# Performance work log

Hardware: AMD Instinct MI355X
Metric: run time of the kernel (lower is better)

The kernel has to match this reference:

```python
import jax, jax.numpy as jnp
import numpy as np

# ---- constants matching the torch module / entmax normmax_bisect defaults ----
ALPHA = 5.0                 # normmax alpha (entmax normmax_bisect default)
N_BISECT = 50               # bisection iterations
K_EXP = 1.0 / (ALPHA - 1.0)        # p_i propto (z_i - tau)_+^{1/(alpha-1)}
AK_EXP = ALPHA / (ALPHA - 1.0)     # norm condition: sum (z-tau)_+^{alpha/(alpha-1)} = 1
EPS = 1e-8                  # module epsilon
LN_EPS = 1e-5               # torch LayerNorm default eps

B, N, C, D = 32, 1024, 64, 768


def _bisect_tau(z):
    # z: [..., S]; find tau with f(tau) = sum_i relu(z_i - tau)^AK_EXP - 1 = 0 (f decreasing)
    max_val = jnp.max(z, axis=-1, keepdims=True)
    lo, hi = max_val - 1.0, max_val  # f(lo) >= 0, f(hi) = -1 < 0

    def body(_, carry):
        lo, hi = carry
        tau = 0.5 * (lo + hi)
        f = jnp.sum(jnp.maximum(z - tau, 0.0) ** AK_EXP, axis=-1, keepdims=True) - 1.0
        lo = jnp.where(f >= 0, tau, lo)
        hi = jnp.where(f >= 0, hi, tau)
        return (lo, hi)

    lo, hi = jax.lax.fori_loop(0, N_BISECT, body, (lo, hi))
    return 0.5 * (lo + hi)


def normmax_last(z):
    # normmax over last axis: p = s / sum(s), s = relu(z - tau)^{1/(alpha-1)}, ||s||_alpha = 1
    tau = _bisect_tau(z)
    u = jnp.maximum(z - tau, 0.0)
    u_safe = jnp.where(u > 0, u, 1.0)
    s = jnp.where(u > 0, u_safe ** K_EXP, 0.0)
    return s / jnp.sum(s, axis=-1, keepdims=True)


def layernorm(x, scale, bias):
    mu = jnp.mean(x, axis=-1, keepdims=True)
    var = jnp.mean((x - mu) ** 2, axis=-1, keepdims=True)
    return (x - mu) * jax.lax.rsqrt(var + LN_EPS) * scale + bias


def setup_inputs() -> dict:
    key = jax.random.key(0)
    ks = jax.random.split(key, 10)
    w = lambda k, shp: (jax.random.normal(k, shp, dtype=jnp.float32) * 0.02)
    return {
        "features": jax.random.normal(ks[0], (B, N, D), dtype=jnp.float32),
        "slots_init": jax.random.normal(ks[1], (B, C, D), dtype=jnp.float32),
        "mask": jax.random.randint(ks[2], (B, N), 0, 2, dtype=jnp.int32),
        "ln_f_scale": jnp.ones((D,), jnp.float32),
        "ln_f_bias": jnp.zeros((D,), jnp.float32),
        "ln_s_scale": jnp.ones((D,), jnp.float32),
        "ln_s_bias": jnp.zeros((D,), jnp.float32),
        "Wk": w(ks[3], (D, D)),
        "Wv": w(ks[4], (D, D)),
        "Wq": w(ks[5], (D, D)),
        "W_ih": w(ks[6], (3 * D, D)),
        "W_hh": w(ks[7], (3 * D, D)),
        "b_ih": jnp.zeros((3 * D,), jnp.float32),
        "b_hh": jnp.zeros((3 * D,), jnp.float32),
    }


def reference(features, slots_init, mask, ln_f_scale, ln_f_bias, ln_s_scale, ln_s_bias,
              Wk, Wv, Wq, W_ih, W_hh, b_ih, b_hh):
    f = layernorm(features, ln_f_scale, ln_f_bias)        # [B,N,D]
    k = f @ Wk.T
    v = f @ Wv.T
    b, n, d = v.shape
    c = slots_init.shape[1]
    m = mask[:, None, :] != 0                             # [B,1,N], broadcasts over C

    # num_iterations = 1; straight-through (detach trick) is the identity here.
    slots_prev = slots_init
    s = layernorm(slots_init, ln_s_scale, ln_s_bias)
    q = s @ Wq.T                                          # [B,C,D]
    logits = jnp.einsum('bcd,bnd->bcn', q, k) * (1.0 / np.sqrt(d))
    logits = jnp.where(m, logits, 0.0)                    # masked_fill(mask==0, 0)
    # normmax over the slot axis (dim=1)
    attn = jnp.moveaxis(normmax_last(jnp.moveaxis(logits, 1, -1)), -1, 1)  # [B,C,N]
    attn = jnp.where(m, attn, 0.0)
    attn_wm = attn / (jnp.sum(attn, axis=-1, keepdims=True) + EPS)
    updates = jnp.einsum('bcn,bnd->bcd', attn_wm, v)      # [B,C,D]

    # torch GRUCell: r,z,n gate order
    x = updates.reshape(-1, d)
    h = slots_prev.reshape(-1, d)
    gi = x @ W_ih.T + b_ih
    gh = h @ W_hh.T + b_hh
    ir, iz, in_ = jnp.split(gi, 3, axis=-1)
    hr, hz, hn = jnp.split(gh, 3, axis=-1)
    r = jax.nn.sigmoid(ir + hr)
    zg = jax.nn.sigmoid(iz + hz)
    ng = jnp.tanh(in_ + r * hn)
    h_new = (1.0 - zg) * ng + zg * h
    slots = h_new.reshape(b, c, d)
    return slots, attn
```

## Files before the change

kernel.cpp:

```cpp
#include <hip/hip_runtime.h>
#include <cstdint>
#include <cmath>

#define DEVINL __device__ __forceinline__

using f32x4  = __attribute__((ext_vector_type(4))) float;
using bf16x8 = __attribute__((ext_vector_type(8))) __bf16;
using u16x8  = __attribute__((ext_vector_type(8))) unsigned short;
using u16x4  = __attribute__((ext_vector_type(4))) unsigned short;
using fl4    = __attribute__((ext_vector_type(4))) float;

DEVINL float bf2f(unsigned short h) {
    unsigned int u = ((unsigned int)h) << 16;
    float f; __builtin_memcpy(&f, &u, 4); return f;
}
DEVINL unsigned short f2bf(float f) {
    unsigned int u; __builtin_memcpy(&u, &f, 4);
    u += 0x7FFFu + ((u >> 16) & 1u);
    return (unsigned short)(u >> 16);
}
DEVINL float sqrt_raw(float x) {
    float r; asm("v_sqrt_f32 %0, %1" : "=v"(r) : "v"(x)); return r;
}

DEVINL void gload_lds16(const unsigned short* g, unsigned short* l) {
    __builtin_amdgcn_global_load_lds(
        (__attribute__((address_space(1))) void*)g,
        (__attribute__((address_space(3))) void*)l,
        16, 0, 0);
}

__global__ __launch_bounds__(256)
void tr2_f2b_split(const float* __restrict__ Wq, const float* __restrict__ Wk,
                   unsigned short* __restrict__ WqT_hi, unsigned short* __restrict__ WqT_lo,
                   unsigned short* __restrict__ WkT_hi, unsigned short* __restrict__ WkT_lo)
{
    constexpr int S = 768 * 768;
    const int o = blockIdx.x * 256 + threadIdx.x;
    if (o >= 2 * S) return;
    const float* x; unsigned short *yh, *yl; int i;
    if (o < S) { x = Wq; yh = WqT_hi; yl = WqT_lo; i = o; }
    else       { x = Wk; yh = WkT_hi; yl = WkT_lo; i = o - S; }
    const int e = i / 768, d = i - e * 768;
    const float v = x[d * 768 + e];
    const unsigned short h = f2bf(v);
    yh[i] = h;
    yl[i] = f2bf(v - bf2f(h));
}

__global__ __launch_bounds__(256)
void conv2_fused(const float* __restrict__ Wih, const float* __restrict__ Whh,
                 const float* __restrict__ sl,  const float* __restrict__ Wv,
                 unsigned short* __restrict__ Wihb, unsigned short* __restrict__ Whhb,
                 unsigned short* __restrict__ slb,  unsigned short* __restrict__ Wvb)
{
    constexpr int S1 = 3 * 768 * 768;
    constexpr int S2 = S1 + 3 * 768 * 768;
    constexpr int S3 = S2 + 32 * 64 * 768;
    constexpr int S4 = S3 + 768 * 768;
    const int i = (blockIdx.x * 256 + threadIdx.x) * 4;
    if (i >= S4) return;
    const float* src; unsigned short* dst; int off;
    if (i < S1)      { src = Wih; dst = Wihb; off = i; }
    else if (i < S2) { src = Whh; dst = Whhb; off = i - S1; }
    else if (i < S3) { src = sl;  dst = slb;  off = i - S2; }
    else             { src = Wv;  dst = Wvb;  off = i - S3; }
    fl4 v = *(const fl4*)(src + off);
    u16x4 o;
#pragma unroll
    for (int j = 0; j < 4; ++j) o[j] = f2bf(v[j]);
    *(u16x4*)(dst + off) = o;
}

template<int BM, int BN, int WAVES_M, int WAVES_N, int OUTMODE>
__global__ __launch_bounds__(256)
void gemm_bt3(const unsigned short* __restrict__ Ah, const unsigned short* __restrict__ Al,
              const unsigned short* __restrict__ Bh, const unsigned short* __restrict__ Bl,
              void* __restrict__ out1, unsigned short* __restrict__ out2,
              int N, int K, long sA, long sB, long sC, float alpha)
{
    constexpr int BK = 32;
    constexpr int WM = BM / WAVES_M, WN = BN / WAVES_N;
    constexpr int MT = WM / 16, NT = WN / 16;
    __shared__ alignas(16) unsigned short Ash[BM * BK], Asl[BM * BK];
    __shared__ alignas(16) unsigned short Bsh[BN * BK], Bsl[BN * BK];

    const int bz = blockIdx.z;
    Ah += (long)bz * sA; Al += (long)bz * sA;
    Bh += (long)bz * sB; Bl += (long)bz * sB;
    const int row0 = blockIdx.y * BM, col0 = blockIdx.x * BN;
    const int tid = threadIdx.x, l = tid & 63, w = tid >> 6;
    const int wm = w / WAVES_N, wn = w % WAVES_N;
    const int fr = l & 15, fq = l >> 4;

    f32x4 acc[MT][NT] = {};
    constexpr int ACALLS = (BM * BK) / (256 * 8);
    constexpr int BCALLS = (BN * BK) / (256 * 8);

    for (int kt = 0; kt < K; kt += BK) {
#pragma unroll
        for (int c = 0; c < ACALLS; ++c) {
            const int e = (c * 256 + tid) * 8;
            const long g = (long)(row0 + (e >> 5)) * K + kt + (e & 31);
            gload_lds16(Ah + g, &Ash[e]);
            gload_lds16(Al + g, &Asl[e]);
        }
#pragma unroll
        for (int c = 0; c < BCALLS; ++c) {
            const int e = (c * 256 + tid) * 8;
            const long g = (long)(col0 + (e >> 5)) * K + kt + (e & 31);
            gload_lds16(Bh + g, &Bsh[e]);
            gload_lds16(Bl + g, &Bsl[e]);
        }
        __syncthreads();

        bf16x8 afh[MT], afl[MT], bfh[NT], bfl[NT];
#pragma unroll
        for (int m = 0; m < MT; ++m) {
            const int o = (wm * WM + m * 16 + fr) * BK + fq * 8;
            afh[m] = __builtin_bit_cast(bf16x8, *(const u16x8*)&Ash[o]);
            afl[m] = __builtin_bit_cast(bf16x8, *(const u16x8*)&Asl[o]);
        }
#pragma unroll
        for (int n = 0; n < NT; ++n) {
            const int o = (wn * WN + n * 16 + fr) * BK + fq * 8;
            bfh[n] = __builtin_bit_cast(bf16x8, *(const u16x8*)&Bsh[o]);
            bfl[n] = __builtin_bit_cast(bf16x8, *(const u16x8*)&Bsl[o]);
        }
#pragma unroll
        for (int m = 0; m < MT; ++m)
#pragma unroll
            for (int n = 0; n < NT; ++n) {
                acc[m][n] = __builtin_amdgcn_mfma_f32_16x16x32_bf16(afh[m], bfh[n], acc[m][n], 0, 0, 0);
                acc[m][n] = __builtin_amdgcn_mfma_f32_16x16x32_bf16(afh[m], bfl[n], acc[m][n], 0, 0, 0);
                acc[m][n] = __builtin_amdgcn_mfma_f32_16x16x32_bf16(afl[m], bfh[n], acc[m][n], 0, 0, 0);
            }
        __syncthreads();
    }

#pragma unroll
    for (int m = 0; m < MT; ++m) {
        const int gr = row0 + wm * WM + m * 16 + fq * 4;
#pragma unroll
        for (int n = 0; n < NT; ++n) {
            const int gc = col0 + wn * WN + n * 16 + fr;
#pragma unroll
            for (int j = 0; j < 4; ++j) {
                const float v = acc[m][n][j] * alpha;
                const long idx = (long)bz * sC + (long)(gr + j) * N + gc;
                if (OUTMODE == 0) {
                    ((float*)out1)[idx] = v;
                } else {
                    const unsigned short h = f2bf(v);
                    ((unsigned short*)out1)[idx] = h;
                    out2[idx] = f2bf(v - bf2f(h));
                }
            }
        }
    }
}

template<int BM, int BN, int WAVES_M, int WAVES_N, bool OUT_F32>
__global__ __launch_bounds__(256)
void gemm_bt(const unsigned short* __restrict__ A,
             const unsigned short* __restrict__ B,
             void* __restrict__ Cv,
             int N, int K, long sA, long sB, long sC, float alpha)
{
    constexpr int BK = 32;
    constexpr int WM = BM / WAVES_M, WN = BN / WAVES_N;
    constexpr int MT = WM / 16, NT = WN / 16;
    __shared__ alignas(16) unsigned short As[BM * BK];
    __shared__ alignas(16) unsigned short Bs[BN * BK];

    const int bz = blockIdx.z;
    A += (long)bz * sA;
    B += (long)bz * sB;
    const int row0 = blockIdx.y * BM, col0 = blockIdx.x * BN;
    const int tid = threadIdx.x, l = tid & 63, w = tid >> 6;
    const int wm = w / WAVES_N, wn = w % WAVES_N;
    const int fr = l & 15, fq = l >> 4;

    f32x4 acc[MT][NT] = {};
    constexpr int ACALLS = (BM * BK) / (256 * 8);
    constexpr int BCALLS = (BN * BK) / (256 * 8);

    for (int kt = 0; kt < K; kt += BK) {
#pragma unroll
        for (int c = 0; c < ACALLS; ++c) {
            const int e = (c * 256 + tid) * 8;
            gload_lds16(A + (long)(row0 + (e >> 5)) * K + kt + (e & 31), &As[e]);
        }
#pragma unroll
        for (int c = 0; c < BCALLS; ++c) {
            const int e = (c * 256 + tid) * 8;
            gload_lds16(B + (long)(col0 + (e >> 5)) * K + kt + (e & 31), &Bs[e]);
        }
        __syncthreads();

        bf16x8 af[MT], bfr[NT];
#pragma unroll
        for (int m = 0; m < MT; ++m)
            af[m] = __builtin_bit_cast(bf16x8, *(const u16x8*)&As[(wm * WM + m * 16 + fr) * BK + fq * 8]);
#pragma unroll
        for (int n = 0; n < NT; ++n)
            bfr[n] = __builtin_bit_cast(bf16x8, *(const u16x8*)&Bs[(wn * WN + n * 16 + fr) * BK + fq * 8]);
#pragma unroll
        for (int m = 0; m < MT; ++m)
#pragma unroll
            for (int n = 0; n < NT; ++n)
                acc[m][n] = __builtin_amdgcn_mfma_f32_16x16x32_bf16(af[m], bfr[n], acc[m][n], 0, 0, 0);
        __syncthreads();
    }

#pragma unroll
    for (int m = 0; m < MT; ++m) {
        const int gr = row0 + wm * WM + m * 16 + fq * 4;
#pragma unroll
        for (int n = 0; n < NT; ++n) {
            const int gc = col0 + wn * WN + n * 16 + fr;
#pragma unroll
            for (int j = 0; j < 4; ++j) {
                const float v = acc[m][n][j] * alpha;
                if (OUT_F32) ((float*)Cv)[(long)bz * sC + (long)(gr + j) * N + gc] = v;
                else ((unsigned short*)Cv)[(long)bz * sC + (long)(gr + j) * N + gc] = f2bf(v);
            }
        }
    }
}

template<int BM, int BN, int WAVES_M, int WAVES_N>
__global__ __launch_bounds__(256)
void gemm_nt_rs(const unsigned short* __restrict__ A,
                const unsigned short* __restrict__ Bm,
                unsigned short* __restrict__ C,
                int N, int K, long sA, long sB, long sC)
{
    constexpr int BK = 32;
    constexpr int WM = BM / WAVES_M, WN = BN / WAVES_N;
    constexpr int MT = WM / 16, NT = WN / 16;
    __shared__ alignas(16) unsigned short As[BM * BK];
    __shared__ alignas(16) unsigned short Bs[BN * BK];
    __shared__ float rsums[BM];

    const int bz = blockIdx.z;
    A += (long)bz * sA;
    Bm += (long)bz * sB;
    const int row0 = blockIdx.y * BM, col0 = blockIdx.x * BN;
    const int tid = threadIdx.x, l = tid & 63, w = tid >> 6;
    const int wm = w / WAVES_N, wn = w % WAVES_N;
    const int fr = l & 15, fq = l >> 4;

    f32x4 acc[MT][NT] = {};
    float rsum = 0.f;
    constexpr int ACALLS = (BM * BK) / (256 * 8);
    constexpr int TPR = BN / 8;
    constexpr int RPP = 256 / TPR;
    const int br = tid / TPR, bc8 = (tid % TPR) * 8;

    for (int kt = 0; kt < K; kt += BK) {
#pragma unroll
        for (int c = 0; c < ACALLS; ++c) {
            const int e = (c * 256 + tid) * 8;
            gload_lds16(A + (long)(row0 + (e >> 5)) * K + kt + (e & 31), &As[e]);
        }
#pragma unroll
        for (int p = 0; p < BK / RPP; ++p) {
            const int r = p * RPP + br;
            u16x8 vv = *(const u16x8*)(Bm + (long)(kt + r) * N + col0 + bc8);
#pragma unroll
            for (int j = 0; j < 8; ++j) Bs[(bc8 + j) * BK + r] = vv[j];
        }
        __syncthreads();

        if (tid < BM) {
#pragma unroll
            for (int kk = 0; kk < BK / 8; ++kk) {
                u16x8 vv = *(const u16x8*)&As[tid * BK + kk * 8];
#pragma unroll
                for (int j = 0; j < 8; ++j) rsum += bf2f(vv[j]);
            }
        }

        bf16x8 af[MT], bfr[NT];
#pragma unroll
        for (int m = 0; m < MT; ++m)
            af[m] = __builtin_bit_cast(bf16x8, *(const u16x8*)&As[(wm * WM + m * 16 + fr) * BK + fq * 8]);
#pragma unroll
        for (int n = 0; n < NT; ++n)
            bfr[n] = __builtin_bit_cast(bf16x8, *(const u16x8*)&Bs[(wn * WN + n * 16 + fr) * BK + fq * 8]);
#pragma unroll
        for (int m = 0; m < MT; ++m)
#pragma unroll
            for (int n = 0; n < NT; ++n)
                acc[m][n] = __builtin_amdgcn_mfma_f32_16x16x32_bf16(af[m], bfr[n], acc[m][n], 0, 0, 0);
        __syncthreads();
    }

    if (tid < BM) rsums[tid] = rsum;
    __syncthreads();

#pragma unroll
    for (int m = 0; m < MT; ++m) {
        const int lr = wm * WM + m * 16 + fq * 4;
        const int gr = row0 + lr;
#pragma unroll
        for (int n = 0; n < NT; ++n) {
            const int gc = col0 + wn * WN + n * 16 + fr;
#pragma unroll
            for (int j = 0; j < 4; ++j) {
                const float inv = 1.f / (rsums[lr + j] + 1e-8f);
                C[(long)bz * sC + (long)(gr + j) * N + gc] = f2bf(acc[m][n][j] * inv);
            }
        }
    }
}

__global__ __launch_bounds__(256)
void ln_fused(const float* __restrict__ xf, const float* __restrict__ gf,
              const float* __restrict__ bf,
              unsigned short* __restrict__ fh, unsigned short* __restrict__ fl,
              const float* __restrict__ xs, const float* __restrict__ gs,
              const float* __restrict__ bs,
              unsigned short* __restrict__ sh, unsigned short* __restrict__ sl,
              int nrows_f)
{
    constexpr int D = 768;
    const int lane = threadIdx.x & 63;
    long row = (long)blockIdx.x * 4 + (threadIdx.x >> 6);
    const float *x, *g, *bb_;
    unsigned short *yh, *yl;
    if (row < nrows_f) { x = xf; g = gf; bb_ = bf; yh = fh; yl = fl; }
    else { row -= nrows_f; x = xs; g = gs; bb_ = bs; yh = sh; yl = sl; }

    const float* xr = x + row * D;
    float v[12];
#pragma unroll
    for (int p = 0; p < 3; ++p) {
        fl4 t = *(const fl4*)(xr + p * 256 + lane * 4);
#pragma unroll
        for (int j = 0; j < 4; ++j) v[p * 4 + j] = t[j];
    }
    float s = 0.f, s2 = 0.f;
#pragma unroll
    for (int j = 0; j < 12; ++j) { s += v[j]; s2 += v[j] * v[j]; }
#pragma unroll
    for (int o = 1; o < 64; o <<= 1) { s += __shfl_xor(s, o); s2 += __shfl_xor(s2, o); }
    const float mu  = s / (float)D;
    const float var = s2 / (float)D - mu * mu;
    const float r   = rsqrtf(var + 1e-5f);

#pragma unroll
    for (int p = 0; p < 3; ++p) {
        fl4 gg = *(const fl4*)(g + p * 256 + lane * 4);
        fl4 be = *(const fl4*)(bb_ + p * 256 + lane * 4);
        u16x4 oh, ol;
#pragma unroll
        for (int j = 0; j < 4; ++j) {
            const float y = (v[p * 4 + j] - mu) * r * gg[j] + be[j];
            oh[j] = f2bf(y);
            ol[j] = f2bf(y - bf2f(oh[j]));
        }
        *(u16x4*)(yh + row * D + p * 256 + lane * 4) = oh;
        *(u16x4*)(yl + row * D + p * 256 + lane * 4) = ol;
    }
}

__global__ __launch_bounds__(256)
void normmax_cols(const float* __restrict__ logits, const int* __restrict__ mask,
                  float* __restrict__ attn_f32, unsigned short* __restrict__ attn_b16)
{
    constexpr int N = 1024, C = 64;
    const int b = blockIdx.y;
    const int tid = threadIdx.x, l = tid & 63, w = tid >> 6;
    const int n = blockIdx.x * 64 + w * 16 + (l & 15);
    const int cb = (l >> 4) * 16;
    const long base = (long)b * C * N + n;
    const float* Lb = logits + base;
    const int m = mask[b * N + n];

    float z[16];
#pragma unroll
    for (int i = 0; i < 16; ++i) z[i] = m ? Lb[(cb + i) * N] : 0.f;

    float mx = z[0];
#pragma unroll
    for (int i = 1; i < 16; ++i) mx = fmaxf(mx, z[i]);
    mx = fmaxf(mx, __shfl_xor(mx, 16));
    mx = fmaxf(mx, __shfl_xor(mx, 32));

    float lo = mx - 1.f, hi = mx;
    for (int it = 0; it < 34; ++it) {
        const float tau = 0.5f * (lo + hi);
        float f = 0.f;
#pragma unroll
        for (int i = 0; i < 16; ++i) {
            const float u = fmaxf(z[i] - tau, 0.f);
            f += u * sqrt_raw(sqrt_raw(u));
        }
        f += __shfl_xor(f, 16);
        f += __shfl_xor(f, 32);
        if (f >= 1.f) lo = tau; else hi = tau;
    }
    const float tau = 0.5f * (lo + hi);
    float sv[16]; float ss = 0.f;
#pragma unroll
    for (int i = 0; i < 16; ++i) {
        const float u = fmaxf(z[i] - tau, 0.f);
        sv[i] = sqrt_raw(sqrt_raw(u));
        ss += sv[i];
    }
    ss += __shfl_xor(ss, 16);
    ss += __shfl_xor(ss, 32);
    const float inv = 1.f / ss;
#pragma unroll
    for (int i = 0; i < 16; ++i) {
        const float a = m ? sv[i] * inv : 0.f;
        attn_f32[base + (long)(cb + i) * N] = a;
        attn_b16[base + (long)(cb + i) * N] = f2bf(a);
    }
}

__global__ __launch_bounds__(256)
void gru_gates(const float* __restrict__ gi, const float* __restrict__ gh,
               const float* __restrict__ b_ih, const float* __restrict__ b_hh,
               const float* __restrict__ h, float* __restrict__ out)
{
    constexpr int D = 768;
    const int t = blockIdx.x * 256 + threadIdx.x;
    const int row = t / (D / 4), d = (t - row * (D / 4)) * 4;
    const float* gir = gi + (long)row * 3 * D;
    const float* ghr = gh + (long)row * 3 * D;
    fl4 ir  = *(const fl4*)(gir + d);
    fl4 iz  = *(const fl4*)(gir + D + d);
    fl4 in_ = *(const fl4*)(gir + 2 * D + d);
    fl4 hr  = *(const fl4*)(ghr + d);
    fl4 hz  = *(const fl4*)(ghr + D + d);
    fl4 hn  = *(const fl4*)(ghr + 2 * D + d);
    fl4 bir = *(const fl4*)(b_ih + d);
    fl4 biz = *(const fl4*)(b_ih + D + d);
    fl4 bin = *(const fl4*)(b_ih + 2 * D + d);
    fl4 bhr = *(const fl4*)(b_hh + d);
    fl4 bhz = *(const fl4*)(b_hh + D + d);
    fl4 bhn = *(const fl4*)(b_hh + 2 * D + d);
    fl4 hv  = *(const fl4*)(h + (long)row * D + d);
    fl4 o;
#pragma unroll
    for (int j = 0; j < 4; ++j) {
        const float r  = 1.f / (1.f + expf(-(ir[j] + bir[j] + hr[j] + bhr[j])));
        const float zg = 1.f / (1.f + expf(-(iz[j] + biz[j] + hz[j] + bhz[j])));
        const float ng = tanhf(in_[j] + bin[j] + r * (hn[j] + bhn[j]));
        o[j] = (1.f - zg) * ng + zg * hv[j];
    }
    *(fl4*)(out + (long)row * D + d) = o;
}

extern "C" void kernel_launch(void* const* d_in, const int* in_sizes, int n_in,
                              void* d_out, int out_size, void* d_ws, size_t ws_size,
                              hipStream_t stream)
{
    const float* features = (const float*)d_in[0];
    const float* slots    = (const float*)d_in[1];
    const int*   mask     = (const int*)d_in[2];
    const float* lnf_g = (const float*)d_in[3];
    const float* lnf_b = (const float*)d_in[4];
    const float* lns_g = (const float*)d_in[5];
    const float* lns_b = (const float*)d_in[6];
    const float* Wk  = (const float*)d_in[7];
    const float* Wv  = (const float*)d_in[8];
    const float* Wq  = (const float*)d_in[9];
    const float* Wih = (const float*)d_in[10];
    const float* Whh = (const float*)d_in[11];
    const float* bih = (const float*)d_in[12];
    const float* bhh = (const float*)d_in[13];

    constexpr int B = 32, N = 1024, C = 64, D = 768;
    char* ws = (char*)d_ws;
    unsigned short* f_hi = (unsigned short*)(ws + 0);
    float*          gi   = (float*)(ws + 0);
    float*          gh   = (float*)(ws + 18874368);
    unsigned short* Wihb = (unsigned short*)(ws + 37748736);
    unsigned short* Whhb = (unsigned short*)(ws + 41287680);
    unsigned short* Wvb  = (unsigned short*)(ws + 44826624);
    unsigned short* f_lo = (unsigned short*)(ws + 50331648);
    unsigned short* ab16 = (unsigned short*)(ws + 50331648);
    unsigned short* Pbf  = (unsigned short*)(ws + 54525952);
    unsigned short* updb = (unsigned short*)(ws + 57671680);
    unsigned short* slb  = (unsigned short*)(ws + 60817408);
    float*          lg     = (float*)(ws + 100663296);
    unsigned short* s_hi   = (unsigned short*)(ws + 109051904);
    unsigned short* s_lo   = (unsigned short*)(ws + 112197632);
    unsigned short* qk_hi  = (unsigned short*)(ws + 115343360);
    unsigned short* qk_lo  = (unsigned short*)(ws + 118489088);
    unsigned short* WqT_hi = (unsigned short*)(ws + 121634816);
    unsigned short* WqT_lo = (unsigned short*)(ws + 122814464);
    unsigned short* WkT_hi = (unsigned short*)(ws + 123994112);
    unsigned short* WkT_lo = (unsigned short*)(ws + 125173760);
    unsigned short* MT_hi  = (unsigned short*)(ws + 126353408);
    unsigned short* MT_lo  = (unsigned short*)(ws + 127533056);

    float* out_slots = (float*)d_out;
    float* out_attn  = out_slots + (long)B * C * D;

    tr2_f2b_split<<<(2 * D * D + 255) / 256, 256, 0, stream>>>(
        Wq, Wk, WqT_hi, WqT_lo, WkT_hi, WkT_lo);

    ln_fused<<<(B * N + B * C) / 4, 256, 0, stream>>>(
        features, lnf_g, lnf_b, f_hi, f_lo,
        slots, lns_g, lns_b, s_hi, s_lo, B * N);

    gemm_bt3<64, 64, 2, 2, 1><<<dim3(D / 64, D / 64, 1), 256, 0, stream>>>(
        WkT_hi, WkT_lo, WqT_hi, WqT_lo, MT_hi, MT_lo, D, D, 0, 0, 0, 1.f);
    gemm_bt3<64, 64, 2, 2, 1><<<dim3(D / 64, (B * C) / 64, 1), 256, 0, stream>>>(
        s_hi, s_lo, MT_hi, MT_lo, qk_hi, qk_lo, D, D, 0, 0, 0, 1.f);
    gemm_bt3<64, 64, 2, 2, 0><<<dim3(N / 64, 1, B), 256, 0, stream>>>(
        qk_hi, qk_lo, f_hi, f_lo, lg, nullptr,
        N, D, (long)C * D, (long)N * D, (long)C * N, 0.03608439182435161f);

    normmax_cols<<<dim3(N / 64, B), 256, 0, stream>>>(lg, mask, out_attn, ab16);

    gemm_nt_rs<64, 64, 2, 2><<<dim3(D / 64, 1, B), 256, 0, stream>>>(
        ab16, f_hi, Pbf, D, N, (long)C * N, (long)N * D, (long)C * D);

    {
        constexpr int TOT = 3 * D * D + 3 * D * D + B * C * D + D * D;
        conv2_fused<<<(TOT / 4 + 255) / 256, 256, 0, stream>>>(
            Wih, Whh, slots, Wv, Wihb, Whhb, slb, Wvb);
    }

    gemm_bt<64, 64, 2, 2, false><<<dim3(D / 64, (B * C) / 64, 1), 256, 0, stream>>>(
        Pbf, Wvb, updb, D, D, 0, 0, 0, 1.f);

    gemm_bt<128, 128, 2, 2, true><<<dim3(3 * D / 128, (B * C) / 128, 2), 256, 0, stream>>>(
        updb, Wihb, gi, 3 * D, D,
        (long)(B * C) * D, (long)(3 * D) * D, (long)(B * C) * 3 * D, 1.f);

    gru_gates<<<(B * C * D / 4) / 256, 256, 0, stream>>>(gi, gh, bih, bhh, slots, out_slots);
}
```

Measured before the change: 224.7 us.

## Interleave bf16 hi/lo split halves per row into a single buffer

The separate hi and lo bf16 buffers for features, slots, q-k products and weight transposes are merged into one row-interleaved buffer, with each row holding D hi values followed by D lo values. All GEMM loaders, the LN kernel and the transpose kernel are updated to address this layout, and the LN kernel now writes 8-wide vectors. The aim is better locality and fewer distinct memory streams and pages per tile load. The workspace aliasing is also reshuffled, which risks overlaps between buffers that are still live.

Measured after the change: 227.1 us. Within noise of the previous version (+1.0%).

```diff
diff --git a/kernel.cpp b/kernel.cpp
--- a/kernel.cpp
+++ b/kernel.cpp
@@ -3,6 +3,7 @@
 #include <cmath>
 
 #define DEVINL __device__ __forceinline__
+
 
 using f32x4  = __attribute__((ext_vector_type(4))) float;
 using bf16x8 = __attribute__((ext_vector_type(8))) __bf16;
@@ -32,20 +33,19 @@
 
 __global__ __launch_bounds__(256)
 void tr2_f2b_split(const float* __restrict__ Wq, const float* __restrict__ Wk,
-                   unsigned short* __restrict__ WqT_hi, unsigned short* __restrict__ WqT_lo,
-                   unsigned short* __restrict__ WkT_hi, unsigned short* __restrict__ WkT_lo)
+                   unsigned short* __restrict__ WqT_i, unsigned short* __restrict__ WkT_i)
 {
     constexpr int S = 768 * 768;
     const int o = blockIdx.x * 256 + threadIdx.x;
     if (o >= 2 * S) return;
-    const float* x; unsigned short *yh, *yl; int i;
-    if (o < S) { x = Wq; yh = WqT_hi; yl = WqT_lo; i = o; }
-    else       { x = Wk; yh = WkT_hi; yl = WkT_lo; i = o - S; }
+    const float* x; unsigned short* y; int i;
+    if (o < S) { x = Wq; y = WqT_i; i = o; }
+    else       { x = Wk; y = WkT_i; i = o - S; }
     const int e = i / 768, d = i - e * 768;
     const float v = x[d * 768 + e];
     const unsigned short h = f2bf(v);
-    yh[i] = h;
-    yl[i] = f2bf(v - bf2f(h));
+    y[(long)e * 1536 + d]       = h;
+    y[(long)e * 1536 + 768 + d] = f2bf(v - bf2f(h));
 }
 
 __global__ __launch_bounds__(256)
@@ -74,9 +74,8 @@
 
 template<int BM, int BN, int WAVES_M, int WAVES_N, int OUTMODE>
 __global__ __launch_bounds__(256)
-void gemm_bt3(const unsigned short* __restrict__ Ah, const unsigned short* __restrict__ Al,
-              const unsigned short* __restrict__ Bh, const unsigned short* __restrict__ Bl,
-              void* __restrict__ out1, unsigned short* __restrict__ out2,
+void gemm_bt3(const unsigned short* __restrict__ AB, const unsigned short* __restrict__ BB,
+              void* __restrict__ out1,
               int N, int K, long sA, long sB, long sC, float alpha)
 {
     constexpr int BK = 32;
@@ -86,8 +85,8 @@
     __shared__ alignas(16) unsigned short Bsh[BN * BK], Bsl[BN * BK];
 
     const int bz = blockIdx.z;
-    Ah += (long)bz * sA; Al += (long)bz * sA;
-    Bh += (long)bz * sB; Bl += (long)bz * sB;
+    AB += (long)bz * sA;
+    BB += (long)bz * sB;
     const int row0 = blockIdx.y * BM, col0 = blockIdx.x * BN;
     const int tid = threadIdx.x, l = tid & 63, w = tid >> 6;
     const int wm = w / WAVES_N, wn = w % WAVES_N;
@@ -101,16 +100,16 @@
 #pragma unroll
         for (int c = 0; c < ACALLS; ++c) {
             const int e = (c * 256 + tid) * 8;
-            const long g = (long)(row0 + (e >> 5)) * K + kt + (e & 31);
-            gload_lds16(Ah + g, &Ash[e]);
-            gload_lds16(Al + g, &Asl[e]);
+            const long rb = (long)(row0 + (e >> 5)) * (2 * K) + kt + (e & 31);
+            gload_lds16(AB + rb, &Ash[e]);
+            gload_lds16(AB + rb + K, &Asl[e]);
         }
 #pragma unroll
         for (int c = 0; c < BCALLS; ++c) {
             const int e = (c * 256 + tid) * 8;
-            const long g = (long)(col0 + (e >> 5)) * K + kt + (e & 31);
-            gload_lds16(Bh + g, &Bsh[e]);
-            gload_lds16(Bl + g, &Bsl[e]);
+            const long rb = (long)(col0 + (e >> 5)) * (2 * K) + kt + (e & 31);
+            gload_lds16(BB + rb, &Bsh[e]);
+            gload_lds16(BB + rb + K, &Bsl[e]);
         }
         __syncthreads();
 
@@ -147,13 +146,14 @@
 #pragma unroll
             for (int j = 0; j < 4; ++j) {
                 const float v = acc[m][n][j] * alpha;
-                const long idx = (long)bz * sC + (long)(gr + j) * N + gc;
                 if (OUTMODE == 0) {
-                    ((float*)out1)[idx] = v;
+                    ((float*)out1)[(long)bz * sC + (long)(gr + j) * N + gc] = v;
                 } else {
+                    unsigned short* ob = (unsigned short*)out1;
+                    const long rb = (long)(gr + j) * (2 * N) + gc;
                     const unsigned short h = f2bf(v);
-                    ((unsigned short*)out1)[idx] = h;
-                    out2[idx] = f2bf(v - bf2f(h));
+                    ob[rb] = h;
+                    ob[rb + N] = f2bf(v - bf2f(h));
                 }
             }
         }
@@ -267,7 +267,7 @@
 #pragma unroll
         for (int p = 0; p < BK / RPP; ++p) {
             const int r = p * RPP + br;
-            u16x8 vv = *(const u16x8*)(Bm + (long)(kt + r) * N + col0 + bc8);
+            u16x8 vv = *(const u16x8*)(Bm + (long)(kt + r) * (2 * N) + col0 + bc8);
 #pragma unroll
             for (int j = 0; j < 8; ++j) Bs[(bc8 + j) * BK + r] = vv[j];
         }
@@ -319,50 +319,79 @@
 __global__ __launch_bounds__(256)
 void ln_fused(const float* __restrict__ xf, const float* __restrict__ gf,
               const float* __restrict__ bf,
-              unsigned short* __restrict__ fh, unsigned short* __restrict__ fl,
+              unsigned short* __restrict__ fi,
               const float* __restrict__ xs, const float* __restrict__ gs,
               const float* __restrict__ bs,
-              unsigned short* __restrict__ sh, unsigned short* __restrict__ sl,
+              unsigned short* __restrict__ si,
               int nrows_f)
 {
     constexpr int D = 768;
     const int lane = threadIdx.x & 63;
     long row = (long)blockIdx.x * 4 + (threadIdx.x >> 6);
     const float *x, *g, *bb_;
-    unsigned short *yh, *yl;
-    if (row < nrows_f) { x = xf; g = gf; bb_ = bf; yh = fh; yl = fl; }
-    else { row -= nrows_f; x = xs; g = gs; bb_ = bs; yh = sh; yl = sl; }
+    unsigned short* y;
+    if (row < nrows_f) { x = xf; g = gf; bb_ = bf; y = fi; }
+    else { row -= nrows_f; x = xs; g = gs; bb_ = bs; y = si; }
 
     const float* xr = x + row * D;
-    float v[12];
-#pragma unroll
-    for (int p = 0; p < 3; ++p) {
-        fl4 t = *(const fl4*)(xr + p * 256 + lane * 4);
-#pragma unroll
-        for (int j = 0; j < 4; ++j) v[p * 4 + j] = t[j];
+    const int eA = lane * 8;
+    const int eB = 512 + lane * 8;
+    float v[16];
+    {
+        fl4 a = *(const fl4*)(xr + eA);
+        fl4 b = *(const fl4*)(xr + eA + 4);
+#pragma unroll
+        for (int j = 0; j < 4; ++j) { v[j] = a[j]; v[4 + j] = b[j]; }
+    }
+    if (lane < 32) {
+        fl4 a = *(const fl4*)(xr + eB);
+        fl4 b = *(const fl4*)(xr + eB + 4);
+#pragma unroll
+        for (int j = 0; j < 4; ++j) { v[8 + j] = a[j]; v[12 + j] = b[j]; }
     }
     float s = 0.f, s2 = 0.f;
 #pragma unroll
-    for (int j = 0; j < 12; ++j) { s += v[j]; s2 += v[j] * v[j]; }
+    for (int j = 0; j < 8; ++j) { s += v[j]; s2 += v[j] * v[j]; }
+    if (lane < 32) {
+#pragma unroll
+        for (int j = 8; j < 16; ++j) { s += v[j]; s2 += v[j] * v[j]; }
+    }
 #pragma unroll
     for (int o = 1; o < 64; o <<= 1) { s += __shfl_xor(s, o); s2 += __shfl_xor(s2, o); }
     const float mu  = s / (float)D;
     const float var = s2 / (float)D - mu * mu;
     const float r   = rsqrtf(var + 1e-5f);
 
-#pragma unroll
-    for (int p = 0; p < 3; ++p) {
-        fl4 gg = *(const fl4*)(g + p * 256 + lane * 4);
-        fl4 be = *(const fl4*)(bb_ + p * 256 + lane * 4);
-        u16x4 oh, ol;
-#pragma unroll
-        for (int j = 0; j < 4; ++j) {
-            const float y = (v[p * 4 + j] - mu) * r * gg[j] + be[j];
-            oh[j] = f2bf(y);
-            ol[j] = f2bf(y - bf2f(oh[j]));
-        }
-        *(u16x4*)(yh + row * D + p * 256 + lane * 4) = oh;
-        *(u16x4*)(yl + row * D + p * 256 + lane * 4) = ol;
+    unsigned short* yr = y + row * (2 * D);
+    {
+        fl4 g0 = *(const fl4*)(g + eA), g1 = *(const fl4*)(g + eA + 4);
+        fl4 b0 = *(const fl4*)(bb_ + eA), b1 = *(const fl4*)(bb_ + eA + 4);
+        u16x8 oh, ol;
+#pragma unroll
+        for (int j = 0; j < 8; ++j) {
+            const float gg = (j < 4) ? g0[j] : g1[j - 4];
+            const float be = (j < 4) ? b0[j] : b1[j - 4];
+            const float yv = (v[j] - mu) * r * gg + be;
+            oh[j] = f2bf(yv);
+            ol[j] = f2bf(yv - bf2f(oh[j]));
+        }
+        *(u16x8*)(yr + eA) = oh;
+        *(u16x8*)(yr + D + eA) = ol;
+    }
+    if (lane < 32) {
+        fl4 g0 = *(const fl4*)(g + eB), g1 = *(const fl4*)(g + eB + 4);
+        fl4 b0 = *(const fl4*)(bb_ + eB), b1 = *(const fl4*)(bb_ + eB + 4);
+        u16x8 oh, ol;
+#pragma unroll
+        for (int j = 0; j < 8; ++j) {
+            const float gg = (j < 4) ? g0[j] : g1[j - 4];
+            const float be = (j < 4) ? b0[j] : b1[j - 4];
+            const float yv = (v[8 + j] - mu) * r * gg + be;
+            oh[j] = f2bf(yv);
+            ol[j] = f2bf(yv - bf2f(oh[j]));
+        }
+        *(u16x8*)(yr + eB) = oh;
+        *(u16x8*)(yr + D + eB) = ol;
     }
 }
 
@@ -476,51 +505,44 @@
 
     constexpr int B = 32, N = 1024, C = 64, D = 768;
     char* ws = (char*)d_ws;
-    unsigned short* f_hi = (unsigned short*)(ws + 0);
+    unsigned short* f_i  = (unsigned short*)(ws + 0);
     float*          gi   = (float*)(ws + 0);
     float*          gh   = (float*)(ws + 18874368);
     unsigned short* Wihb = (unsigned short*)(ws + 37748736);
     unsigned short* Whhb = (unsigned short*)(ws + 41287680);
     unsigned short* Wvb  = (unsigned short*)(ws + 44826624);
-    unsigned short* f_lo = (unsigned short*)(ws + 50331648);
-    unsigned short* ab16 = (unsigned short*)(ws + 50331648);
-    unsigned short* Pbf  = (unsigned short*)(ws + 54525952);
     unsigned short* updb = (unsigned short*)(ws + 57671680);
     unsigned short* slb  = (unsigned short*)(ws + 60817408);
     float*          lg     = (float*)(ws + 100663296);
-    unsigned short* s_hi   = (unsigned short*)(ws + 109051904);
-    unsigned short* s_lo   = (unsigned short*)(ws + 112197632);
-    unsigned short* qk_hi  = (unsigned short*)(ws + 115343360);
-    unsigned short* qk_lo  = (unsigned short*)(ws + 118489088);
-    unsigned short* WqT_hi = (unsigned short*)(ws + 121634816);
-    unsigned short* WqT_lo = (unsigned short*)(ws + 122814464);
-    unsigned short* WkT_hi = (unsigned short*)(ws + 123994112);
-    unsigned short* WkT_lo = (unsigned short*)(ws + 125173760);
-    unsigned short* MT_hi  = (unsigned short*)(ws + 126353408);
-    unsigned short* MT_lo  = (unsigned short*)(ws + 127533056);
+    unsigned short* s_i    = (unsigned short*)(ws + 109051904);
+    unsigned short* ab16   = (unsigned short*)(ws + 109051904);
+    unsigned short* qk_i   = (unsigned short*)(ws + 115343360);
+    unsigned short* Pbf    = (unsigned short*)(ws + 115343360);
+    unsigned short* WqT_i  = (unsigned short*)(ws + 121634816);
+    unsigned short* WkT_i  = (unsigned short*)(ws + 123994112);
+    unsigned short* M_i    = (unsigned short*)(ws + 126353408);
 
     float* out_slots = (float*)d_out;
     float* out_attn  = out_slots + (long)B * C * D;
 
-    tr2_f2b_split<<<(2 * D * D + 255) / 256, 256, 0, stream>>>(
-        Wq, Wk, WqT_hi, WqT_lo, WkT_hi, WkT_lo);
+    tr2_f2b_split<<<(2 * D * D + 255) / 256, 256, 0, stream>>>(Wq, Wk, WqT_i, WkT_i);
 
     ln_fused<<<(B * N + B * C) / 4, 256, 0, stream>>>(
-        features, lnf_g, lnf_b, f_hi, f_lo,
-        slots, lns_g, lns_b, s_hi, s_lo, B * N);
+        features, lnf_g, lnf_b, f_i,
+        slots, lns_g, lns_b, s_i, B * N);
 
     gemm_bt3<64, 64, 2, 2, 1><<<dim3(D / 64, D / 64, 1), 256, 0, stream>>>(
-        WkT_hi, WkT_lo, WqT_hi, WqT_lo, MT_hi, MT_lo, D, D, 0, 0, 0, 1.f);
+        WkT_i, WqT_i, M_i, D, D, 0, 0, 0, 1.f);
     gemm_bt3<64, 64, 2, 2, 1><<<dim3(D / 64, (B * C) / 64, 1), 256, 0, stream>>>(
-        s_hi, s_lo, MT_hi, MT_lo, qk_hi, qk_lo, D, D, 0, 0, 0, 1.f);
+        s_i, M_i, qk_i, D, D, 0, 0, 0, 1.f);
     gemm_bt3<64, 64, 2, 2, 0><<<dim3(N / 64, 1, B), 256, 0, stream>>>(
-        qk_hi, qk_lo, f_hi, f_lo, lg, nullptr,
-        N, D, (long)C * D, (long)N * D, (long)C * N, 0.03608439182435161f);
+        qk_i, f_i, lg,
+        N, D, (long)C * 2 * D, (long)N * 2 * D, (long)C * N, 0.03608439182435161f);
 
     normmax_cols<<<dim3(N / 64, B), 256, 0, stream>>>(lg, mask, out_attn, ab16);
 
     gemm_nt_rs<64, 64, 2, 2><<<dim3(D / 64, 1, B), 256, 0, stream>>>(
-        ab16, f_hi, Pbf, D, N, (long)C * N, (long)N * D, (long)C * D);
+        ab16, f_i, Pbf, D, N, (long)C * N, (long)N * 2 * D, (long)C * D);
 
     {
         constexpr int TOT = 3 * D * D + 3 * D * D + B * C * D + D * D;
```
